# Kernel tuning notes

Measured on AMD Instinct MI355X. Metric: run time of the kernel, lower is better.

The kernel has to match this reference:

```python
import jax, jax.numpy as jnp
import numpy as np
from jax import lax

DN3 = ('NDHWC', 'DHWIO', 'NDHWC')
DN2 = ('NHWC', 'HWIO', 'NHWC')


def conv3d(x, w, b, s):
    return lax.conv_general_dilated(x, w, s, 'VALID', dimension_numbers=DN3) + b


def deconv3d(x, w, b, s):
    # Keras Conv3DTranspose, padding='valid': out = (in-1)*stride + kernel
    return lax.conv_transpose(x, w, s, 'VALID', dimension_numbers=DN3) + b


def conv2d_same(x, w):
    return lax.conv_general_dilated(x, w, (1, 1), 'SAME', dimension_numbers=DN2)


def hard_sigmoid(x):
    # Keras ConvLSTM2D default recurrent_activation
    return jnp.clip(0.2 * x + 0.5, 0.0, 1.0)


def convlstm2d(xseq, wx, wh, b):
    # xseq: (B, T, H, W, Cin); wx: (3,3,Cin,4F); wh: (3,3,F,4F); b: (4F,)
    # Inference mode: dropout / recurrent_dropout are identity.
    B, T, H, W, _ = xseq.shape
    F = wh.shape[2]
    xs = jnp.moveaxis(xseq, 1, 0)  # (T, B, H, W, Cin)
    h0 = jnp.zeros((B, H, W, F), xseq.dtype)
    c0 = jnp.zeros((B, H, W, F), xseq.dtype)

    def step(carry, xt):
        h, c = carry
        z = conv2d_same(xt, wx) + conv2d_same(h, wh) + b
        i, f, g, o = jnp.split(z, 4, axis=-1)  # Keras gate order i,f,c,o
        c = hard_sigmoid(f) * c + hard_sigmoid(i) * jnp.tanh(g)
        h = hard_sigmoid(o) * jnp.tanh(c)
        return (h, c), h

    _, hs = lax.scan(step, (h0, c0), xs)
    return jnp.moveaxis(hs, 0, 1)  # (B, T, H, W, F)


def setup_inputs() -> dict:
    key = jax.random.key(0)
    ks = jax.random.split(key, 18)
    g = lambda k, shape, fan: (jax.random.normal(k, shape, jnp.float32) / np.sqrt(fan)).astype(jnp.float32)
    inp = {
        'x': jax.random.normal(ks[0], (8, 227, 227, 10, 1), jnp.float32),
        # encoder Conv3D
        'c1w': g(ks[1], (11, 11, 1, 1, 128), 11 * 11 * 1), 'c1b': jnp.zeros((128,), jnp.float32),
        'c2w': g(ks[2], (5, 5, 1, 128, 64), 5 * 5 * 128), 'c2b': jnp.zeros((64,), jnp.float32),
        # ConvLSTM2D stack (64 -> 32 -> 64 filters)
        'l1x': g(ks[3], (3, 3, 64, 256), 9 * 64), 'l1h': g(ks[4], (3, 3, 64, 256), 9 * 64), 'l1b': jnp.zeros((256,), jnp.float32),
        'l2x': g(ks[5], (3, 3, 64, 128), 9 * 64), 'l2h': g(ks[6], (3, 3, 32, 128), 9 * 32), 'l2b': jnp.zeros((128,), jnp.float32),
        'l3x': g(ks[7], (3, 3, 32, 256), 9 * 32), 'l3h': g(ks[8], (3, 3, 64, 256), 9 * 64), 'l3b': jnp.zeros((256,), jnp.float32),
        # decoder Conv3DTranspose
        'd1w': g(ks[9], (5, 5, 1, 64, 128), 5 * 5 * 64), 'd1b': jnp.zeros((128,), jnp.float32),
        'd2w': g(ks[10], (11, 11, 1, 128, 1), 11 * 11 * 128), 'd2b': jnp.zeros((1,), jnp.float32),
    }
    return inp


def reference(x, c1w, c1b, c2w, c2b, l1x, l1h, l1b, l2x, l2h, l2b,
              l3x, l3h, l3b, d1w, d1b, d2w, d2b):
    e = jax.nn.relu(conv3d(x, c1w, c1b, (4, 4, 1)))   # (B,55,55,10,128)
    e = jax.nn.relu(conv3d(e, c2w, c2b, (2, 2, 1)))   # (B,26,26,10,64)
    # encoded tensor fed straight into ConvLSTM2D: time=26, rows=26, cols=10
    h = convlstm2d(e, l1x, l1h, l1b)                  # (B,26,26,10,64)
    h = convlstm2d(h, l2x, l2h, l2b)                  # (B,26,26,10,32)
    h = convlstm2d(h, l3x, l3h, l3b)                  # (B,26,26,10,64)
    d = jax.nn.relu(deconv3d(h, d1w, d1b, (2, 2, 1)))  # (B,55,55,10,128)
    d = jax.nn.relu(deconv3d(d, d2w, d2b, (4, 4, 1)))  # (B,227,227,10,1)
    return d
```

## Files before the change

kernel.cpp:

```cpp
#include <hip/hip_runtime.h>
#include <math.h>


__device__ __forceinline__ float hsig(float x) {
    float y = 0.2f * x + 0.5f;
    return fminf(fmaxf(y, 0.f), 1.f);
}

__global__ __launch_bounds__(256) void k_conv1(const float* __restrict__ x,
                                               const float* __restrict__ w1,
                                               const float* __restrict__ b1,
                                               float* __restrict__ e1) {
    int bid = blockIdx.x;
    int ht = bid & 3; int tmp = bid >> 2;
    int w = tmp % 10; tmp /= 10;
    int d = tmp % 55; int n = tmp / 55;
    int h0 = ht * 16;

    __shared__ __align__(16) float patch[11][72];
    int tid = threadIdx.x;
    for (int idx = tid; idx < 11 * 71; idx += 256) {
        int j = idx % 71; int kd = idx / 71;
        int rr = d * 4 + kd; int cc = h0 * 4 + j;
        float v = 0.f;
        if (cc < 227) v = x[((n * 227 + rr) * 227 + cc) * 10 + w];
        patch[kd][j] = v;
    }
    __syncthreads();

    int co = tid & 127, pg = tid >> 7;
    float acc[8];
#pragma unroll
    for (int p = 0; p < 8; p++) acc[p] = 0.f;

    for (int kd = 0; kd < 11; kd++) {
        const float4* row = (const float4*)&patch[kd][pg * 32];
        float rr2[40];
#pragma unroll
        for (int q = 0; q < 10; q++) {
            float4 t4 = row[q];
            rr2[4 * q] = t4.x; rr2[4 * q + 1] = t4.y; rr2[4 * q + 2] = t4.z; rr2[4 * q + 3] = t4.w;
        }
        const float* wp = w1 + (kd * 11) * 128 + co;
#pragma unroll
        for (int kh = 0; kh < 11; kh++) {
            float wv = wp[kh * 128];
#pragma unroll
            for (int p = 0; p < 8; p++) acc[p] += rr2[p * 4 + kh] * wv;
        }
    }
    float bv = b1[co];
#pragma unroll
    for (int p = 0; p < 8; p++) {
        int h = h0 + pg * 8 + p;
        if (h < 55)
            e1[(((n * 55 + d) * 55 + h) * 10 + w) * 128 + co] = fmaxf(acc[p] + bv, 0.f);
    }
}

__global__ __launch_bounds__(256) void k_conv2(const float* __restrict__ e1,
                                               const float* __restrict__ w2,
                                               const float* __restrict__ b2,
                                               float* __restrict__ e2) {
    int bid = (blockIdx.x & 7) * 260 + (blockIdx.x >> 3);
    int w = bid % 10; int tmp = bid / 10;
    int d = tmp % 26; int n = tmp / 26;

    __shared__ __align__(16) float patch[5][16][60];
    int tid = threadIdx.x;
    int co = tid & 63, pg = tid >> 6;
    int hb = pg * 7;
    int np = (pg == 3) ? 5 : 7;
    int base = pg * 14;
    float bv = b2[co];
    float acc[7];
#pragma unroll
    for (int p = 0; p < 7; p++) acc[p] = bv;

    for (int c0 = 0; c0 < 128; c0 += 16) {
        __syncthreads();
        for (int idx = tid; idx < 5 * 59 * 16; idx += 256) {
            int ci = idx & 15; int t2 = idx >> 4;
            int col = t2 % 59; int kr = t2 / 59;
            float v = 0.f;
            if (col < 55)
                v = e1[(((n * 55 + d * 2 + kr) * 55 + col) * 10 + w) * 128 + c0 + ci];
            patch[kr][ci][col] = v;
        }
        __syncthreads();

        for (int kr = 0; kr < 5; kr++) {
            for (int ci0 = 0; ci0 < 16; ci0 += 4) {
                float wv[4][5];
#pragma unroll
                for (int u = 0; u < 4; u++) {
                    const float* wp = w2 + ((kr * 5) * 128 + c0 + ci0 + u) * 64 + co;
#pragma unroll
                    for (int kh = 0; kh < 5; kh++) wv[u][kh] = wp[kh * 128 * 64];
                }
#pragma unroll
                for (int u = 0; u < 4; u++) {
                    const float* pr = &patch[kr][ci0 + u][base];
                    float rr2[18];
#pragma unroll
                    for (int q = 0; q < 9; q++) {
                        float2 t2v = *(const float2*)(pr + 2 * q);
                        rr2[2 * q] = t2v.x; rr2[2 * q + 1] = t2v.y;
                    }
#pragma unroll
                    for (int kh = 0; kh < 5; kh++) {
                        float w_ = wv[u][kh];
#pragma unroll
                        for (int p = 0; p < 7; p++)
                            acc[p] += rr2[2 * p + kh] * w_;
                    }
                }
            }
        }
    }
#pragma unroll
    for (int p = 0; p < 7; p++) {
        if (p < np) {
            int h = hb + p;
            e2[(((n * 26 + d) * 26 + h) * 10 + w) * 64 + co] = fmaxf(acc[p], 0.f);
        }
    }
}

template <int CIN, int COUT>
__global__ __launch_bounds__(COUT) void k_xconv(const float* __restrict__ in,
                                                const float* __restrict__ wx,
                                                const float* __restrict__ bias,
                                                float* __restrict__ xz) {
    int bid = blockIdx.x;
    int r = bid % 26; int fr = bid / 26;
    int n = fr / 26, t = fr % 26;

    __shared__ __align__(16) float patch[3][CIN][12];
    int tid = threadIdx.x;
    const float* inf = in + (size_t)fr * (26 * 10 * CIN);
    for (int idx = tid; idx < 3 * 12 * CIN; idx += COUT) {
        int ci = idx % CIN; int t2 = idx / CIN;
        int col = t2 % 12; int kr = t2 / 12;
        int rr = r - 1 + kr; int cc = col - 1;
        float v = 0.f;
        if (rr >= 0 && rr < 26 && cc >= 0 && cc < 10)
            v = inf[(rr * 10 + cc) * CIN + ci];
        patch[kr][ci][col] = v;
    }
    __syncthreads();

    int co = tid;
    float bv = bias[co];
    float acc[10];
#pragma unroll
    for (int c = 0; c < 10; c++) acc[c] = bv;

    for (int kr = 0; kr < 3; kr++) {
        for (int ci0 = 0; ci0 < CIN; ci0 += 4) {
            float wv[4][3];
#pragma unroll
            for (int u = 0; u < 4; u++) {
                const float* wp = wx + ((kr * 3) * CIN + ci0 + u) * COUT + co;
#pragma unroll
                for (int kc = 0; kc < 3; kc++) wv[u][kc] = wp[kc * CIN * COUT];
            }
#pragma unroll
            for (int u = 0; u < 4; u++) {
                const float4* row = (const float4*)&patch[kr][ci0 + u][0];
                float rr2[12];
#pragma unroll
                for (int q = 0; q < 3; q++) {
                    float4 t4 = row[q];
                    rr2[4 * q] = t4.x; rr2[4 * q + 1] = t4.y;
                    rr2[4 * q + 2] = t4.z; rr2[4 * q + 3] = t4.w;
                }
#pragma unroll
                for (int kc = 0; kc < 3; kc++) {
                    float w_ = wv[u][kc];
#pragma unroll
                    for (int c = 0; c < 10; c++) acc[c] += rr2[c + kc] * w_;
                }
            }
        }
    }
    float* outp = xz + ((size_t)(t * 8 + n) * 260 + r * 10) * COUT + co;
#pragma unroll
    for (int c = 0; c < 10; c++) outp[c * COUT] = acc[c];
}

__global__ void k_rst(int* __restrict__ f) {
    if (threadIdx.x < 208)
        __hip_atomic_store(f + threadIdx.x, 0, __ATOMIC_RELAXED,
                           __HIP_MEMORY_SCOPE_AGENT);
}

template <int F, int QS>
__global__ __launch_bounds__(4 * F * QS) void k_lstm(const float* __restrict__ xz,
                                                     const float* __restrict__ wh,
                                                     float* __restrict__ y,
                                                     int* __restrict__ flags) {
    constexpr int C4 = 4 * F;
    constexpr int NT = 4 * F * QS;
    constexpr int CQ = F / QS;
    int bid = blockIdx.x;
    int r = bid % 26; int b = bid / 26;
    int tid = threadIdx.x;
    int co = tid & (C4 - 1);
    int q = tid / C4;
    int ci0 = q * CQ;

    __shared__ __align__(16) float patch[3][F][12];
    __shared__ float zpart[QS][10][C4];

    for (int i = tid; i < 3 * F * 12; i += NT) ((float*)patch)[i] = 0.f;
    __syncthreads();

    float creg = 0.f;
    int gc = tid / F, gf = tid % F;
    int* fl = flags + b * 26;

    for (int t = 0; t < 26; t++) {
        if (t > 0) {
            if (tid < 2) {
                int nb = (tid == 0) ? r - 1 : r + 1;
                if (nb >= 0 && nb < 26) {
                    while (__hip_atomic_load(fl + nb, __ATOMIC_RELAXED,
                                             __HIP_MEMORY_SCOPE_AGENT) < t)
                        __builtin_amdgcn_s_sleep(1);
                }
            }
            __syncthreads();

            for (int i = tid; i < 2 * 10 * F; i += NT) {
                int ci = i % F; int t2 = i / F;
                int col = t2 % 10; int s = t2 / 10;
                int kr = 2 * s; int rr = r - 1 + kr;
                float v = 0.f;
                if (rr >= 0 && rr < 26)
                    v = __hip_atomic_load(
                        &y[((((size_t)b * 26 + (t - 1)) * 26 + rr) * 10 + col) * F + ci],
                        __ATOMIC_RELAXED, __HIP_MEMORY_SCOPE_AGENT);
                patch[kr][ci][col + 1] = v;
            }
            __syncthreads();
        }

        float acc[10];
        if (q == 0) {
            const float* xp = xz + ((size_t)(t * 8 + b) * 260 + r * 10) * C4 + co;
#pragma unroll
            for (int c = 0; c < 10; c++) acc[c] = xp[c * C4];
        } else {
#pragma unroll
            for (int c = 0; c < 10; c++) acc[c] = 0.f;
        }

        if (t > 0) {
            const int krseq[3] = {1, 0, 2};
            for (int kk = 0; kk < 3; kk++) {
                const int kr = krseq[kk];
                for (int cu = 0; cu < CQ; cu += 4) {
                    float wv[4][3];
#pragma unroll
                    for (int u = 0; u < 4; u++) {
                        const float* wp = wh + ((kr * 3) * F + ci0 + cu + u) * C4 + co;
#pragma unroll
                        for (int kc = 0; kc < 3; kc++) wv[u][kc] = wp[kc * F * C4];
                    }
#pragma unroll
                    for (int u = 0; u < 4; u++) {
                        const float4* row = (const float4*)&patch[kr][ci0 + cu + u][0];
                        float rr2[12];
#pragma unroll
                        for (int v4 = 0; v4 < 3; v4++) {
                            float4 t4 = row[v4];
                            rr2[4 * v4] = t4.x; rr2[4 * v4 + 1] = t4.y;
                            rr2[4 * v4 + 2] = t4.z; rr2[4 * v4 + 3] = t4.w;
                        }
#pragma unroll
                        for (int kc = 0; kc < 3; kc++) {
                            float w_ = wv[u][kc];
#pragma unroll
                            for (int c = 0; c < 10; c++) acc[c] += rr2[c + kc] * w_;
                        }
                    }
                }
            }
        }

#pragma unroll
        for (int c = 0; c < 10; c++) zpart[q][c][co] = acc[c];
        __syncthreads();

        if (tid < 10 * F) {
            float zi = 0.f, zf = 0.f, zg = 0.f, zo = 0.f;
#pragma unroll
            for (int qq = 0; qq < QS; qq++) {
                zi += zpart[qq][gc][gf];
                zf += zpart[qq][gc][F + gf];
                zg += zpart[qq][gc][2 * F + gf];
                zo += zpart[qq][gc][3 * F + gf];
            }
            float cn = hsig(zf) * creg + hsig(zi) * tanhf(zg);
            float hn = hsig(zo) * tanhf(cn);
            creg = cn;
            __hip_atomic_store(
                &y[((((size_t)b * 26 + t) * 26 + r) * 10 + gc) * F + gf], hn,
                __ATOMIC_RELAXED, __HIP_MEMORY_SCOPE_AGENT);
            patch[1][gf][gc + 1] = hn;
        }
        __syncthreads();

        if (tid == 0)
            __hip_atomic_store(fl + r, t + 1, __ATOMIC_RELEASE,
                               __HIP_MEMORY_SCOPE_AGENT);
    }
}

__global__ __launch_bounds__(256) void k_deconv1(const float* __restrict__ h3,
                                                 const float* __restrict__ dw,
                                                 const float* __restrict__ db,
                                                 float* __restrict__ out) {
    int bid = blockIdx.x;
    int ht = bid & 1; int tmp = bid >> 1;
    int w = tmp % 10; tmp /= 10;
    int od = tmp % 55; int n = tmp / 55;

    __shared__ __align__(16) float patch[3][64][24];
    int tid = threadIdx.x;
    int odd = od & 1;
    int id0 = odd ? (od - 3) / 2 : od / 2 - 2;
    int ihb = ht * 16 - 2;
    for (int idx = tid; idx < 3 * 20 * 64; idx += 256) {
        int ci = idx & 63; int t2 = idx >> 6;
        int j = t2 % 20; int s = t2 / 20;
        int id = id0 + s; int ih = ihb + j;
        float v = 0.f;
        if (id >= 0 && id < 26 && ih >= 0 && ih < 26)
            v = h3[((((size_t)n * 26 + id) * 26 + ih) * 10 + w) * 64 + ci];
        patch[s][ci][j] = v;
    }
    __syncthreads();

    int co = tid & 127, pg = tid >> 7;
    float acc[16];
#pragma unroll
    for (int p = 0; p < 16; p++) acc[p] = 0.f;

    int nslot = odd ? 2 : 3;
    for (int s = 0; s < nslot; s++) {
        int kd = odd ? (1 + 2 * s) : 2 * s;
        for (int ci = 0; ci < 64; ci++) {
            const float* pr = &patch[s][ci][pg * 8];
            float rr2[10];
            {
                float4 t0 = *(const float4*)pr;
                float4 t1 = *(const float4*)(pr + 4);
                float2 t2v = *(const float2*)(pr + 8);
                rr2[0] = t0.x; rr2[1] = t0.y; rr2[2] = t0.z; rr2[3] = t0.w;
                rr2[4] = t1.x; rr2[5] = t1.y; rr2[6] = t1.z; rr2[7] = t1.w;
                rr2[8] = t2v.x; rr2[9] = t2v.y;
            }
            const float* wp = dw + ((kd * 5) * 64 + ci) * 128 + co;
#pragma unroll
            for (int kh = 0; kh < 5; kh++) {
                float wv = wp[kh * 64 * 128];
                const int po = kh & 1;
                const int rbase = (kh + po) >> 1;
#pragma unroll
                for (int jj = 0; jj < 8; jj++)
                    acc[po + 2 * jj] += rr2[rbase + jj] * wv;
            }
        }
    }
    float bv = db[co];
#pragma unroll
    for (int p = 0; p < 16; p++) {
        int oh = ht * 32 + pg * 16 + p;
        if (oh < 55)
            out[((((size_t)n * 55 + od) * 55 + oh) * 10 + w) * 128 + co] =
                fmaxf(acc[p] + bv, 0.f);
    }
}

__global__ __launch_bounds__(256) void k_dc2_gemm(const float* __restrict__ d1n,
                                                  const float* __restrict__ dw,
                                                  float* __restrict__ Dn) {
    int pix = blockIdx.x * 256 + threadIdx.x;
    bool act = pix < 30250;
    int y = blockIdx.y;
    int k0 = (y == 0) ? 0 : 16 + (y - 1) * 15;
    int kn = (y == 0) ? 16 : 15;

    float a[128];
    const float* ap = d1n + (size_t)(act ? pix : 0) * 128;
#pragma unroll
    for (int i = 0; i < 32; i++) {
        float4 v = ((const float4*)ap)[i];
        a[4 * i] = v.x; a[4 * i + 1] = v.y; a[4 * i + 2] = v.z; a[4 * i + 3] = v.w;
    }

    for (int kk = 0; kk < kn; kk++) {
        int k = k0 + kk;
        const float* wp = dw + k * 128;
        float acc0 = 0.f, acc1 = 0.f, acc2 = 0.f, acc3 = 0.f;
#pragma unroll
        for (int i = 0; i < 32; i++) {
            acc0 += a[4 * i + 0] * wp[4 * i + 0];
            acc1 += a[4 * i + 1] * wp[4 * i + 1];
            acc2 += a[4 * i + 2] * wp[4 * i + 2];
            acc3 += a[4 * i + 3] * wp[4 * i + 3];
        }
        if (act) Dn[k * 30250 + pix] = (acc0 + acc1) + (acc2 + acc3);
    }
}

__global__ __launch_bounds__(256) void k_dc2_scatter(const float* __restrict__ Dn,
                                                     const float* __restrict__ db,
                                                     float* __restrict__ outn) {
    int od = blockIdx.x;
    int pd = od & 3, qd = od >> 2;
    float bv = db[0];
    int p0 = blockIdx.y * 768;
    int p1 = min(2270, p0 + 768);

    for (int p = p0 + threadIdx.x; p < p1; p += 256) {
        int w = p % 10, oh = p / 10;
        int ph = oh & 3, qh = oh >> 2;
        float acc = 0.f;
#pragma unroll
        for (int s = 0; s < 3; s++) {
            int kpd = pd + 4 * s; int id = qd - s;
            if (kpd <= 10 && id >= 0 && id < 55) {
                int kd = 10 - kpd;
#pragma unroll
                for (int t = 0; t < 3; t++) {
                    int kph = ph + 4 * t; int ih = qh - t;
                    if (kph <= 10 && ih >= 0 && ih < 55) {
                        int kh = 10 - kph;
                        acc += Dn[(kd * 11 + kh) * 30250 + (id * 55 + ih) * 10 + w];
                    }
                }
            }
        }
        outn[(size_t)od * 2270 + p] = fmaxf(acc + bv, 0.f);
    }
}

extern "C" void kernel_launch(void* const* d_in, const int* in_sizes, int n_in,
                              void* d_out, int out_size, void* d_ws, size_t ws_size,
                              hipStream_t stream) {
    const float* x   = (const float*)d_in[0];
    const float* c1w = (const float*)d_in[1];
    const float* c1b = (const float*)d_in[2];
    const float* c2w = (const float*)d_in[3];
    const float* c2b = (const float*)d_in[4];
    const float* l1x = (const float*)d_in[5];
    const float* l1h = (const float*)d_in[6];
    const float* l1b = (const float*)d_in[7];
    const float* l2x = (const float*)d_in[8];
    const float* l2h = (const float*)d_in[9];
    const float* l2b = (const float*)d_in[10];
    const float* l3x = (const float*)d_in[11];
    const float* l3h = (const float*)d_in[12];
    const float* l3b = (const float*)d_in[13];
    const float* d1w = (const float*)d_in[14];
    const float* d1b = (const float*)d_in[15];
    const float* d2w = (const float*)d_in[16];
    const float* d2b = (const float*)d_in[17];

    float* ws = (float*)d_ws;
    float* A  = ws;
    float* B  = A + 30976000;
    float* C  = B + 3461120;
    float* S  = C + 3461120;
    float* Y1 = A + 20000000;
    float* Y2 = A + 24000000;
    float* Y3 = C;
    float* D  = B;
    int* FL = (int*)S;
    float* OUT = (float*)d_out;

    k_conv1<<<17600, 256, 0, stream>>>(x, c1w, c1b, A);
    k_conv2<<<2080, 256, 0, stream>>>(A, c2w, c2b, B);

    k_xconv<64, 256><<<208 * 26, 256, 0, stream>>>(B, l1x, l1b, A);
    k_rst<<<1, 256, 0, stream>>>(FL);
    k_lstm<64, 4><<<208, 1024, 0, stream>>>(A, l1h, Y1, FL);

    k_xconv<64, 128><<<208 * 26, 128, 0, stream>>>(Y1, l2x, l2b, A);
    k_rst<<<1, 256, 0, stream>>>(FL);
    k_lstm<32, 8><<<208, 1024, 0, stream>>>(A, l2h, Y2, FL);

    k_xconv<32, 256><<<208 * 26, 256, 0, stream>>>(Y2, l3x, l3b, A);
    k_rst<<<1, 256, 0, stream>>>(FL);
    k_lstm<64, 4><<<208, 1024, 0, stream>>>(A, l3h, Y3, FL);

    k_deconv1<<<8800, 256, 0, stream>>>(Y3, d1w, d1b, A);

    for (int n = 0; n < 8; n++) {
        const float* d1n = A + (size_t)n * 3872000;
        float* outn = OUT + (size_t)n * 515290;
        k_dc2_gemm<<<dim3(119, 8), 256, 0, stream>>>(d1n, d2w, D);
        k_dc2_scatter<<<dim3(227, 3), 256, 0, stream>>>(D, d2b, outn);
    }
}
```

Measured before the change: 3.281 ms.

## Compute own-row recurrent term before waiting on neighbor row flags

In the ConvLSTM wavefront kernel, the contribution of the block's own row (kernel row 1) plus the input term is now computed before spinning on neighbour flags. It is parked in shared memory, and the neighbour rows (kernel rows 0 and 2) are added after the wait and patch load. This hides the inter-block synchronisation latency behind a third of the recurrent FLOPs. It adds an extra shared-memory round trip of the partial sums per step.

```diff
diff --git a/kernel.cpp b/kernel.cpp
--- a/kernel.cpp
+++ b/kernel.cpp
@@ -221,6 +221,49 @@
     int* fl = flags + b * 26;
 
     for (int t = 0; t < 26; t++) {
+        {
+            float acc[10];
+            if (q == 0) {
+                const float* xp = xz + ((size_t)(t * 8 + b) * 260 + r * 10) * C4 + co;
+#pragma unroll
+                for (int c = 0; c < 10; c++) acc[c] = xp[c * C4];
+            } else {
+#pragma unroll
+                for (int c = 0; c < 10; c++) acc[c] = 0.f;
+            }
+            if (t > 0) {
+                const int kr = 1;
+                for (int cu = 0; cu < CQ; cu += 4) {
+                    float wv[4][3];
+#pragma unroll
+                    for (int u = 0; u < 4; u++) {
+                        const float* wp = wh + ((kr * 3) * F + ci0 + cu + u) * C4 + co;
+#pragma unroll
+                        for (int kc = 0; kc < 3; kc++) wv[u][kc] = wp[kc * F * C4];
+                    }
+#pragma unroll
+                    for (int u = 0; u < 4; u++) {
+                        const float4* row = (const float4*)&patch[kr][ci0 + cu + u][0];
+                        float rr2[12];
+#pragma unroll
+                        for (int v4 = 0; v4 < 3; v4++) {
+                            float4 t4 = row[v4];
+                            rr2[4 * v4] = t4.x; rr2[4 * v4 + 1] = t4.y;
+                            rr2[4 * v4 + 2] = t4.z; rr2[4 * v4 + 3] = t4.w;
+                        }
+#pragma unroll
+                        for (int kc = 0; kc < 3; kc++) {
+                            float w_ = wv[u][kc];
+#pragma unroll
+                            for (int c = 0; c < 10; c++) acc[c] += rr2[c + kc] * w_;
+                        }
+                    }
+                }
+            }
+#pragma unroll
+            for (int c = 0; c < 10; c++) zpart[q][c][co] = acc[c];
+        }
+
         if (t > 0) {
             if (tid < 2) {
                 int nb = (tid == 0) ? r - 1 : r + 1;
@@ -244,53 +287,45 @@
                 patch[kr][ci][col + 1] = v;
             }
             __syncthreads();
-        }
-
-        float acc[10];
-        if (q == 0) {
-            const float* xp = xz + ((size_t)(t * 8 + b) * 260 + r * 10) * C4 + co;
-#pragma unroll
-            for (int c = 0; c < 10; c++) acc[c] = xp[c * C4];
-        } else {
-#pragma unroll
-            for (int c = 0; c < 10; c++) acc[c] = 0.f;
-        }
-
-        if (t > 0) {
-            const int krseq[3] = {1, 0, 2};
-            for (int kk = 0; kk < 3; kk++) {
-                const int kr = krseq[kk];
-                for (int cu = 0; cu < CQ; cu += 4) {
-                    float wv[4][3];
-#pragma unroll
-                    for (int u = 0; u < 4; u++) {
-                        const float* wp = wh + ((kr * 3) * F + ci0 + cu + u) * C4 + co;
-#pragma unroll
-                        for (int kc = 0; kc < 3; kc++) wv[u][kc] = wp[kc * F * C4];
-                    }
-#pragma unroll
-                    for (int u = 0; u < 4; u++) {
-                        const float4* row = (const float4*)&patch[kr][ci0 + cu + u][0];
-                        float rr2[12];
-#pragma unroll
-                        for (int v4 = 0; v4 < 3; v4++) {
-                            float4 t4 = row[v4];
-                            rr2[4 * v4] = t4.x; rr2[4 * v4 + 1] = t4.y;
-                            rr2[4 * v4 + 2] = t4.z; rr2[4 * v4 + 3] = t4.w;
+
+            {
+                float acc[10];
+#pragma unroll
+                for (int c = 0; c < 10; c++) acc[c] = zpart[q][c][co];
+                const int krseq2[2] = {0, 2};
+                for (int kk = 0; kk < 2; kk++) {
+                    const int kr = krseq2[kk];
+                    for (int cu = 0; cu < CQ; cu += 4) {
+                        float wv[4][3];
+#pragma unroll
+                        for (int u = 0; u < 4; u++) {
+                            const float* wp = wh + ((kr * 3) * F + ci0 + cu + u) * C4 + co;
+#pragma unroll
+                            for (int kc = 0; kc < 3; kc++) wv[u][kc] = wp[kc * F * C4];
                         }
 #pragma unroll
-                        for (int kc = 0; kc < 3; kc++) {
-                            float w_ = wv[u][kc];
-#pragma unroll
-                            for (int c = 0; c < 10; c++) acc[c] += rr2[c + kc] * w_;
+                        for (int u = 0; u < 4; u++) {
+                            const float4* row = (const float4*)&patch[kr][ci0 + cu + u][0];
+                            float rr2[12];
+#pragma unroll
+                            for (int v4 = 0; v4 < 3; v4++) {
+                                float4 t4 = row[v4];
+                                rr2[4 * v4] = t4.x; rr2[4 * v4 + 1] = t4.y;
+                                rr2[4 * v4 + 2] = t4.z; rr2[4 * v4 + 3] = t4.w;
+                            }
+#pragma unroll
+                            for (int kc = 0; kc < 3; kc++) {
+                                float w_ = wv[u][kc];
+#pragma unroll
+                                for (int c = 0; c < 10; c++) acc[c] += rr2[c + kc] * w_;
+                            }
                         }
                     }
                 }
-            }
-        }
-
-#pragma unroll
-        for (int c = 0; c < 10; c++) zpart[q][c][co] = acc[c];
+#pragma unroll
+                for (int c = 0; c < 10; c++) zpart[q][c][co] = acc[c];
+            }
+        }
         __syncthreads();
 
         if (tid < 10 * F) {
```

Result: slower. 5.654 ms (+72.3%).
